# Performance work log

Measured on AMD Instinct MI355X. Metric: run time of the kernel, lower is better.

## Reference

```python
import jax, jax.numpy as jnp
import numpy as np

H = 2048       # hidden_size
NH = 16        # num query heads
NKV = 4        # num key/value heads
HD = 128       # head_dim
EPS = 1e-6
ROPE_BASE = 10000.0


def rms_norm(x, w):
    xf = x.astype(jnp.float32)
    var = jnp.mean(xf * xf, axis=-1, keepdims=True)
    return (w * (xf * jax.lax.rsqrt(var + EPS)).astype(x.dtype))


def rope_cos_sin(seq_len, dtype):
    inv_freq = 1.0 / (ROPE_BASE ** (jnp.arange(0, HD, 2, dtype=jnp.float32) / HD))
    pos = jnp.arange(seq_len, dtype=jnp.float32)
    ang = pos[:, None] * inv_freq[None, :]            # [S, HD/2]
    emb = jnp.concatenate([ang, ang], axis=-1)        # [S, HD]
    return jnp.cos(emb).astype(dtype), jnp.sin(emb).astype(dtype)


def rotate_half(x):
    x1, x2 = jnp.split(x, 2, axis=-1)
    return jnp.concatenate([-x2, x1], axis=-1)


def setup_inputs() -> dict:
    key = jax.random.key(0)
    ks = jax.random.split(key, 8)
    B, S = 2, 2048
    hidden_states = jax.random.normal(ks[0], (B, S, H), dtype=jnp.float32)
    # additive causal mask [B,1,S,S]
    causal = jnp.where(jnp.tril(jnp.ones((S, S), dtype=bool)), 0.0, -1e9).astype(jnp.float32)
    attention_mask = jnp.broadcast_to(causal[None, None], (B, 1, S, S))
    sc = 1.0 / np.sqrt(H)
    Wq = jax.random.normal(ks[1], (NH * HD, H), dtype=jnp.float32) * sc
    Wk = jax.random.normal(ks[2], (NKV * HD, H), dtype=jnp.float32) * sc
    Wv = jax.random.normal(ks[3], (NKV * HD, H), dtype=jnp.float32) * sc
    Wo = jax.random.normal(ks[4], (H, NH * HD), dtype=jnp.float32) * sc
    q_norm_w = jnp.ones((HD,), dtype=jnp.float32)
    k_norm_w = jnp.ones((HD,), dtype=jnp.float32)
    return {"hidden_states": hidden_states, "attention_mask": attention_mask,
            "Wq": Wq, "Wk": Wk, "Wv": Wv, "Wo": Wo,
            "q_norm_w": q_norm_w, "k_norm_w": k_norm_w}


def reference(hidden_states, attention_mask, Wq, Wk, Wv, Wo, q_norm_w, k_norm_w):
    B, S, _ = hidden_states.shape
    # projections (nn.Linear: x @ W.T)
    q = (hidden_states @ Wq.T).reshape(B, S, NH, HD).transpose(0, 2, 1, 3)   # [B,NH,S,HD]
    k = (hidden_states @ Wk.T).reshape(B, S, NKV, HD).transpose(0, 2, 1, 3)  # [B,NKV,S,HD]
    v = (hidden_states @ Wv.T).reshape(B, S, NKV, HD).transpose(0, 2, 1, 3)
    # QK RMSNorm over head_dim
    q = rms_norm(q, q_norm_w)
    k = rms_norm(k, k_norm_w)
    # RoPE
    cos, sin = rope_cos_sin(S, q.dtype)        # [S,HD]
    q = q * cos + rotate_half(q) * sin
    k = k * cos + rotate_half(k) * sin
    # GQA: repeat kv heads
    n_rep = NH // NKV
    k = jnp.repeat(k, n_rep, axis=1)           # [B,NH,S,HD]
    v = jnp.repeat(v, n_rep, axis=1)
    # attention
    scores = jnp.einsum('bhqd,bhkd->bhqk', q, k) / np.sqrt(HD)
    scores = scores + attention_mask
    probs = jax.nn.softmax(scores, axis=-1)
    attn = jnp.einsum('bhqk,bhkd->bhqd', probs, v)
    attn = attn.transpose(0, 2, 1, 3).reshape(B, S, NH * HD)
    return attn @ Wo.T
```

## Files before the change

kernel.cpp:

```cpp
#include <hip/hip_runtime.h>
#include <hip/hip_bf16.h>
#include <math.h>

#define NH 16
#define NKV 4
#define HD 128
#define SEQ 2048
#define BATCH 2
#define EPSF 1e-6f
#define QKV 3072

typedef __attribute__((ext_vector_type(8))) short bf16x8;
typedef __attribute__((ext_vector_type(4))) short short4v;
typedef __attribute__((ext_vector_type(4))) float f32x4;

__device__ __forceinline__ short f2bf(float x) {
    unsigned u = __float_as_uint(x);
    u += 0x7fffu + ((u >> 16) & 1u);
    return (short)(u >> 16);
}
__device__ __forceinline__ float bf2f(short x) {
    return __uint_as_float((unsigned)(unsigned short)x << 16);
}
__device__ __forceinline__ unsigned pkbf(float a, float b) {
    __hip_bfloat162 h = __float22bfloat162_rn(float2{a, b});
    unsigned r; __builtin_memcpy(&r, &h, 4); return r;
}

__device__ __forceinline__ void gll16(const short* g, short* l) {
    __builtin_amdgcn_global_load_lds(
        (const __attribute__((address_space(1))) unsigned*)g,
        (__attribute__((address_space(3))) unsigned*)l, 16, 0, 0);
}

__global__ __launch_bounds__(256)
void cast_all(const float* __restrict__ hs, const float* __restrict__ Wq,
              const float* __restrict__ Wk, const float* __restrict__ Wv,
              const float* __restrict__ Wo, short* __restrict__ hsb,
              short* __restrict__ wqkv, short* __restrict__ wob,
              float2* __restrict__ rtab)
{
    const size_t MEG = 1024 * 1024;
    const int id = blockIdx.x;
    if (id >= 18432) {
        const int idx = (id - 18432) * 256 + threadIdx.x;
        const int s = idx >> 6, j = idx & 63;
        const float inv_freq = exp2f(-(float)j * (13.287712379549449f / 64.0f));
        const float ang = (float)s * inv_freq;
        float sn, c;
        __sincosf(ang, &sn, &c);
        rtab[idx] = float2{c, sn};
        return;
    }
    const float* s;
    short* d;
    size_t off;
    if (id < 8192)       { s = hs; d = hsb;            off = (size_t)id * 1024; }
    else if (id < 12288) { s = Wq; d = wqkv;           off = (size_t)(id - 8192) * 1024; }
    else if (id < 13312) { s = Wk; d = wqkv + 4 * MEG; off = (size_t)(id - 12288) * 1024; }
    else if (id < 14336) { s = Wv; d = wqkv + 5 * MEG; off = (size_t)(id - 13312) * 1024; }
    else                 { s = Wo; d = wob;            off = (size_t)(id - 14336) * 1024; }
    const size_t i = off + threadIdx.x * 4;
    float4 v = *(const float4*)(s + i);
    short4v o;
    o.x = f2bf(v.x); o.y = f2bf(v.y); o.z = f2bf(v.z); o.w = f2bf(v.w);
    *(short4v*)(d + i) = o;
}

template<bool OUT_BF16>
__global__ __launch_bounds__(256, 4)
void gemm_nt_mfma(const short* __restrict__ A, const short* __restrict__ B,
                  void* __restrict__ Cv, int N, int K, int gridX, int total)
{
    __shared__ short As[128 * 64];
    __shared__ short Bs[128 * 64];

    const int tid = threadIdx.x;
    const int w = tid >> 6, lane = tid & 63;
    const int quad = lane >> 4, ln = lane & 15;
    const int mw = (w >> 1) * 64, nw = (w & 1) * 64;

    const int id = blockIdx.x;
    const int t = (id & 7) * (total >> 3) + (id >> 3);
    const int n0 = (t % gridX) * 128;
    const int m0 = (t / gridX) * 128;

    const int rr = lane >> 3;
    const int gsw = ((lane & 7) ^ rr) * 8;
    const short* Ag[4]; const short* Bg[4];
    short* Al[4]; short* Bl[4];
    #pragma unroll
    for (int r = 0; r < 4; ++r) {
        const int row = w * 8 + 32 * r + rr;
        Ag[r] = A + (size_t)(m0 + row) * K + gsw;
        Bg[r] = B + (size_t)(n0 + row) * K + gsw;
        Al[r] = &As[(w * 8 + 32 * r) * 64];
        Bl[r] = &Bs[(w * 8 + 32 * r) * 64];
    }

    const int col0 = ((quad) ^ (ln & 7)) * 8;
    const int col1 = ((4 + quad) ^ (ln & 7)) * 8;

    f32x4 acc[4][4];
    #pragma unroll
    for (int i = 0; i < 4; ++i)
        #pragma unroll
        for (int j = 0; j < 4; ++j)
            acc[i][j] = (f32x4){0.f, 0.f, 0.f, 0.f};

    for (int k0 = 0; k0 < K; k0 += 64) {
        __syncthreads();
        #pragma unroll
        for (int r = 0; r < 4; ++r) {
            gll16(Ag[r] + k0, Al[r]);
            gll16(Bg[r] + k0, Bl[r]);
        }
        __syncthreads();

        #pragma unroll
        for (int ks = 0; ks < 2; ++ks) {
            const int col = ks ? col1 : col0;
            bf16x8 af[4], bfr[4];
            #pragma unroll
            for (int i = 0; i < 4; ++i)
                af[i] = *(const bf16x8*)&As[(mw + i * 16 + ln) * 64 + col];
            #pragma unroll
            for (int j = 0; j < 4; ++j)
                bfr[j] = *(const bf16x8*)&Bs[(nw + j * 16 + ln) * 64 + col];
            #pragma unroll
            for (int i = 0; i < 4; ++i)
                #pragma unroll
                for (int j = 0; j < 4; ++j)
                    acc[i][j] = __builtin_amdgcn_mfma_f32_16x16x32_bf16(
                        af[i], bfr[j], acc[i][j], 0, 0, 0);
        }
    }

    #pragma unroll
    for (int i = 0; i < 4; ++i) {
        #pragma unroll
        for (int reg = 0; reg < 4; ++reg) {
            const int row = m0 + mw + i * 16 + quad * 4 + reg;
            const size_t base = (size_t)row * N + n0 + nw;
            #pragma unroll
            for (int j = 0; j < 4; ++j) {
                if (OUT_BF16)
                    ((short*)Cv)[base + j * 16 + ln] = f2bf(acc[i][j][reg]);
                else
                    ((float*)Cv)[base + j * 16 + ln] = acc[i][j][reg];
            }
        }
    }
}

#define NR_BLOCKS 20480
__global__ __launch_bounds__(256)
void norm_rope_tv(short* __restrict__ qkv, const float* __restrict__ qw,
                  const float* __restrict__ kw, short* __restrict__ vT,
                  const float2* __restrict__ rtab)
{
    if (blockIdx.x < NR_BLOCKS) {
        const int wave = threadIdx.x >> 6;
        const int lane = threadIdx.x & 63;
        const long vec = (long)blockIdx.x * 4 + wave;
        const long NQ = (long)BATCH * SEQ * NH;

        short* base;
        const float* w;
        int s;
        if (vec < NQ) {
            const long token = vec / NH;
            const int h = (int)(vec % NH);
            s = (int)(token % SEQ);
            base = qkv + token * QKV + h * HD;
            w = qw;
        } else {
            const long t = vec - NQ;
            const long token = t / NKV;
            const int kvh = (int)(t % NKV);
            s = (int)(token % SEQ);
            base = qkv + token * QKV + 2048 + kvh * HD;
            w = kw;
        }

        float x0 = bf2f(base[lane]);
        float x1 = bf2f(base[lane + 64]);
        float ss = x0 * x0 + x1 * x1;
        #pragma unroll
        for (int off = 32; off; off >>= 1) ss += __shfl_xor(ss, off, 64);
        const float r = rsqrtf(ss * (1.0f / HD) + EPSF);
        x0 = x0 * r * w[lane];
        x1 = x1 * r * w[lane + 64];

        const float2 cs = rtab[(size_t)s * 64 + lane];
        base[lane]      = f2bf(x0 * cs.x - x1 * cs.y);
        base[lane + 64] = f2bf(x1 * cs.x + x0 * cs.y);
    } else {
        __shared__ short T[32][33];
        const int bx = blockIdx.x - NR_BLOCKS;
        const int st = bx & 63;
        const int dt = (bx >> 6) & 3;
        const int bk = bx >> 8;
        const int s0 = st * 32, d0 = dt * 32;
        const int tid = threadIdx.x;
        const long tok0 = (long)(bk >> 2) * SEQ + s0;
        const int kvh = bk & 3;

        const int rs = tid >> 3;
        const int rc = (tid & 7) * 4;
        short4v val = *(const short4v*)(qkv + (tok0 + rs) * QKV + 2560 + kvh * HD + d0 + rc);
        T[rc + 0][rs] = val.x; T[rc + 1][rs] = val.y;
        T[rc + 2][rs] = val.z; T[rc + 3][rs] = val.w;
        __syncthreads();

        const int wd = tid >> 3;
        const int wsc = (tid & 7) * 4;
        short4v ov;
        ov.x = T[wd][wsc + 0]; ov.y = T[wd][wsc + 1];
        ov.z = T[wd][wsc + 2]; ov.w = T[wd][wsc + 3];
        *(short4v*)(vT + ((size_t)bk * HD + d0 + wd) * SEQ + s0 + wsc) = ov;
    }
}

__global__ __launch_bounds__(512, 4)
void flash_attn_mfma(const short* __restrict__ qkv, const short* __restrict__ vT,
                     short* __restrict__ o)
{
    __shared__ short Ks[64 * 128];
    __shared__ short Vt[128 * 64];
    __shared__ short Ps[8][16 * 64];

    const int tid = threadIdx.x;
    const int w = tid >> 6;
    const int lane = tid & 63;
    const int quad = lane >> 4;
    const int ln = lane & 15;
    const int lnm = ln & 7;
    const int side = w >> 2;
    const int sw = w & 3;

    const int bx = blockIdx.x;
    const int pair = bx & 15;
    const int bh = bx >> 4;
    const int h = bh & 15;
    const int b = bh >> 4;
    const int kvh = h >> 2;
    const int qa = pair, qb = 31 - pair;
    const int qX = side ? qb : qa;
    const int rX = qX * 64 + sw * 16;

    const float SC = 0.08838834764831845f * 1.4426950408889634f;

    int colK[4];
    #pragma unroll
    for (int f = 0; f < 4; ++f) {
        const int lg = f * 4 + quad;
        colK[f] = ((lg & 8) | ((lg ^ lnm) & 7)) * 8;
    }
    const int colA = (quad ^ lnm) * 8;
    const int colB = ((4 + quad) ^ lnm) * 8;

    bf16x8 qf[4];
    {
        const short* qrow = qkv + (size_t)(b * SEQ + rX + ln) * QKV + h * HD;
        #pragma unroll
        for (int f = 0; f < 4; ++f)
            qf[f] = *(const bf16x8*)(qrow + f * 32 + quad * 8);
    }

    f32x4 Oa[8];
    #pragma unroll
    for (int dg = 0; dg < 8; ++dg) Oa[dg] = (f32x4){0.f, 0.f, 0.f, 0.f};
    float mX = -1e30f, lX = 0.f;

    const short* kbase = qkv + (size_t)(b * SEQ) * QKV + 2048 + kvh * HD;
    const short* vbase = vT + (size_t)(b * NKV + kvh) * HD * SEQ;

    bf16x8 kp[2], vp[2];
    auto prefetch = [&](int k0) {
        #pragma unroll
        for (int i = 0; i < 2; ++i) {
            const int e = tid + i * 512;
            kp[i] = *(const bf16x8*)(kbase + (size_t)(k0 + (e >> 4)) * QKV + (e & 15) * 8);
            vp[i] = *(const bf16x8*)(vbase + (size_t)(e >> 3) * SEQ + k0 + (e & 7) * 8);
        }
    };
    prefetch(0);

    for (int kt = 0; kt <= qb; ++kt) {
        const int k0 = kt * 64;
        __syncthreads();
        #pragma unroll
        for (int i = 0; i < 2; ++i) {
            const int e = tid + i * 512;
            const int kr = e >> 4, kg = e & 15;
            *(bf16x8*)&Ks[kr * 128 + ((kg & 8) | ((kg ^ (kr & 7)) & 7)) * 8] = kp[i];
            const int vd = e >> 3, vg = e & 7;
            *(bf16x8*)&Vt[vd * 64 + ((vg ^ (vd & 7)) * 8)] = vp[i];
        }
        __syncthreads();
        if (kt < qb) prefetch(k0 + 64);

        if (kt <= qX) {
            f32x4 s[4];
            __builtin_amdgcn_s_setprio(1);
            #pragma unroll
            for (int g = 0; g < 4; ++g) {
                f32x4 acc = (f32x4){0.f, 0.f, 0.f, 0.f};
                #pragma unroll
                for (int f = 0; f < 4; ++f) {
                    bf16x8 kf = *(const bf16x8*)&Ks[(g * 16 + ln) * 128 + colK[f]];
                    acc = __builtin_amdgcn_mfma_f32_16x16x32_bf16(kf, qf[f], acc, 0, 0, 0);
                }
                s[g] = acc;
            }
            __builtin_amdgcn_s_setprio(0);
            if (kt == qX) {
                const int qrow = rX + ln;
                #pragma unroll
                for (int g = 0; g < 4; ++g)
                    #pragma unroll
                    for (int reg = 0; reg < 4; ++reg) {
                        const int key = k0 + g * 16 + quad * 4 + reg;
                        if (key > qrow) s[g][reg] = -1e30f;
                    }
            }
            float mt = s[0][0];
            #pragma unroll
            for (int g = 0; g < 4; ++g)
                #pragma unroll
                for (int reg = 0; reg < 4; ++reg)
                    mt = fmaxf(mt, s[g][reg]);
            mt = fmaxf(mt, __shfl_xor(mt, 16, 64));
            mt = fmaxf(mt, __shfl_xor(mt, 32, 64));
            const float mnew = fmaxf(mX, mt);
            const bool defer = __all((mnew - mX) * SC <= 6.0f);
            const float mref = defer ? mX : mnew;
            const float c1 = SC * mref;
            const float alpha = exp2f(__builtin_fmaf(SC, mX, -c1));
            float ps = 0.f;
            #pragma unroll
            for (int g = 0; g < 4; ++g) {
                float p0 = exp2f(__builtin_fmaf(s[g][0], SC, -c1));
                float p1 = exp2f(__builtin_fmaf(s[g][1], SC, -c1));
                float p2 = exp2f(__builtin_fmaf(s[g][2], SC, -c1));
                float p3 = exp2f(__builtin_fmaf(s[g][3], SC, -c1));
                ps += (p0 + p1) + (p2 + p3);
                uint2 pk;
                pk.x = pkbf(p0, p1);
                pk.y = pkbf(p2, p3);
                const int sg = (2 * g + (quad >> 1)) ^ lnm;
                *(uint2*)&Ps[w][ln * 64 + sg * 8 + (quad & 1) * 4] = pk;
            }
            ps += __shfl_xor(ps, 16, 64);
            ps += __shfl_xor(ps, 32, 64);
            mX = mref;
            if (defer) {
                lX += ps;
            } else {
                lX = lX * alpha + ps;
                #pragma unroll
                for (int dg = 0; dg < 8; ++dg) {
                    Oa[dg][0] *= alpha; Oa[dg][1] *= alpha;
                    Oa[dg][2] *= alpha; Oa[dg][3] *= alpha;
                }
            }
            __asm volatile("s_waitcnt lgkmcnt(0)" ::: "memory");
            bf16x8 pf0 = *(const bf16x8*)&Ps[w][ln * 64 + colA];
            bf16x8 pf1 = *(const bf16x8*)&Ps[w][ln * 64 + colB];
            __builtin_amdgcn_s_setprio(1);
            #pragma unroll
            for (int dg = 0; dg < 8; ++dg) {
                bf16x8 vf0 = *(const bf16x8*)&Vt[(dg * 16 + ln) * 64 + colA];
                bf16x8 vf1 = *(const bf16x8*)&Vt[(dg * 16 + ln) * 64 + colB];
                Oa[dg] = __builtin_amdgcn_mfma_f32_16x16x32_bf16(vf0, pf0, Oa[dg], 0, 0, 0);
                Oa[dg] = __builtin_amdgcn_mfma_f32_16x16x32_bf16(vf1, pf1, Oa[dg], 0, 0, 0);
            }
            __builtin_amdgcn_s_setprio(0);
        }
    }

    {
        const float inv = 1.0f / lX;
        short* orow = o + ((size_t)(b * SEQ + rX + ln) * NH + h) * HD;
        #pragma unroll
        for (int dg = 0; dg < 8; ++dg) {
            uint2 ov;
            ov.x = pkbf(Oa[dg][0] * inv, Oa[dg][1] * inv);
            ov.y = pkbf(Oa[dg][2] * inv, Oa[dg][3] * inv);
            *(uint2*)(orow + dg * 16 + quad * 4) = ov;
        }
    }
}

extern "C" void kernel_launch(void* const* d_in, const int* in_sizes, int n_in,
                              void* d_out, int out_size, void* d_ws, size_t ws_size,
                              hipStream_t stream)
{
    const float* hs = (const float*)d_in[0];
    const float* Wq = (const float*)d_in[2];
    const float* Wk = (const float*)d_in[3];
    const float* Wv = (const float*)d_in[4];
    const float* Wo = (const float*)d_in[5];
    const float* qw = (const float*)d_in[6];
    const float* kw = (const float*)d_in[7];
    float* out = (float*)d_out;

    const size_t MEG = 1024 * 1024;
    short* hsb  = (short*)d_ws;
    short* wqkv = hsb + 8 * MEG;
    short* wob  = wqkv + 6 * MEG;
    short* qkvb = wob + 4 * MEG;
    float2* rtab = (float2*)(qkvb + 12 * MEG);
    short* vT   = (short*)d_out;

    dim3 blk(256);

    cast_all<<<dim3(18944), blk, 0, stream>>>(hs, Wq, Wk, Wv, Wo, hsb, wqkv, wob, rtab);

    gemm_nt_mfma<true><<<dim3(768), blk, 0, stream>>>(
        hsb, wqkv, qkvb, QKV, 2048, 24, 768);

    norm_rope_tv<<<dim3(NR_BLOCKS + 2048), blk, 0, stream>>>(qkvb, qw, kw, vT, rtab);

    flash_attn_mfma<<<dim3(512), dim3(512), 0, stream>>>(qkvb, vT, hsb);

    gemm_nt_mfma<false><<<dim3(512), blk, 0, stream>>>(
        hsb, wob, out, 2048, 2048, 16, 512);
}
```

Before: 320.5 us.

## Fuse QK RMSNorm and RoPE into QKV GEMM epilogue

The QKV projection GEMM is split into its own kernel whose warps each own 32 full rows by 128 columns, which is one head per tile. That layout lets the epilogue compute the per-head RMS norm with in-wave shuffles and apply RoPE before writing bf16. This removes the separate norm/rope pass, which reread and rewrote Q and K in global memory. The V transpose becomes its own small kernel. The cost is a changed warp tiling (2x8 accumulators, reloaded B fragments) and a heavier epilogue with strided rtab loads, which may affect GEMM efficiency.

Result: no change. 319.1 us (-0.4%).

```diff
diff --git a/kernel.cpp b/kernel.cpp
--- a/kernel.cpp
+++ b/kernel.cpp
@@ -67,18 +67,19 @@
     *(short4v*)(d + i) = o;
 }
 
-template<bool OUT_BF16>
 __global__ __launch_bounds__(256, 4)
-void gemm_nt_mfma(const short* __restrict__ A, const short* __restrict__ B,
-                  void* __restrict__ Cv, int N, int K, int gridX, int total)
+void gemm_qkv(const short* __restrict__ A, const short* __restrict__ B,
+              short* __restrict__ C, const float* __restrict__ qw,
+              const float* __restrict__ kw, const float2* __restrict__ rtab)
 {
+    const int K = 2048, gridX = 24, total = 768;
     __shared__ short As[128 * 64];
     __shared__ short Bs[128 * 64];
 
     const int tid = threadIdx.x;
     const int w = tid >> 6, lane = tid & 63;
     const int quad = lane >> 4, ln = lane & 15;
-    const int mw = (w >> 1) * 64, nw = (w & 1) * 64;
+    const int lnm = ln & 7;
 
     const int id = blockIdx.x;
     const int t = (id & 7) * (total >> 3) + (id >> 3);
@@ -98,14 +99,14 @@
         Bl[r] = &Bs[(w * 8 + 32 * r) * 64];
     }
 
-    const int col0 = ((quad) ^ (ln & 7)) * 8;
-    const int col1 = ((4 + quad) ^ (ln & 7)) * 8;
-
-    f32x4 acc[4][4];
-    #pragma unroll
-    for (int i = 0; i < 4; ++i)
-        #pragma unroll
-        for (int j = 0; j < 4; ++j)
+    const int col0 = ((quad) ^ lnm) * 8;
+    const int col1 = ((4 + quad) ^ lnm) * 8;
+
+    f32x4 acc[2][8];
+    #pragma unroll
+    for (int i = 0; i < 2; ++i)
+        #pragma unroll
+        for (int j = 0; j < 8; ++j)
             acc[i][j] = (f32x4){0.f, 0.f, 0.f, 0.f};
 
     for (int k0 = 0; k0 < K; k0 += 64) {
@@ -120,6 +121,131 @@
         #pragma unroll
         for (int ks = 0; ks < 2; ++ks) {
             const int col = ks ? col1 : col0;
+            bf16x8 af[2], bq[4];
+            af[0] = *(const bf16x8*)&As[(w * 32 + ln) * 64 + col];
+            af[1] = *(const bf16x8*)&As[(w * 32 + 16 + ln) * 64 + col];
+            #pragma unroll
+            for (int j = 0; j < 4; ++j)
+                bq[j] = *(const bf16x8*)&Bs[(j * 16 + ln) * 64 + col];
+            #pragma unroll
+            for (int i = 0; i < 2; ++i)
+                #pragma unroll
+                for (int j = 0; j < 4; ++j)
+                    acc[i][j] = __builtin_amdgcn_mfma_f32_16x16x32_bf16(
+                        af[i], bq[j], acc[i][j], 0, 0, 0);
+            #pragma unroll
+            for (int j = 0; j < 4; ++j)
+                bq[j] = *(const bf16x8*)&Bs[((j + 4) * 16 + ln) * 64 + col];
+            #pragma unroll
+            for (int i = 0; i < 2; ++i)
+                #pragma unroll
+                for (int j = 0; j < 4; ++j)
+                    acc[i][j + 4] = __builtin_amdgcn_mfma_f32_16x16x32_bf16(
+                        af[i], bq[j], acc[i][j + 4], 0, 0, 0);
+        }
+    }
+
+    const int tn = n0 >> 7;
+    const int rowbase = m0 + w * 32;
+
+    if (tn < 20) {
+        const float* wgt = (tn < 16) ? qw : kw;
+        float wv[8];
+        #pragma unroll
+        for (int j = 0; j < 8; ++j) wv[j] = wgt[j * 16 + ln];
+        #pragma unroll
+        for (int i = 0; i < 2; ++i) {
+            #pragma unroll
+            for (int reg = 0; reg < 4; ++reg) {
+                const int row = rowbase + i * 16 + quad * 4 + reg;
+                const int s = row & (SEQ - 1);
+                float ss = 0.f;
+                #pragma unroll
+                for (int j = 0; j < 8; ++j)
+                    ss += acc[i][j][reg] * acc[i][j][reg];
+                ss += __shfl_xor(ss, 1, 64);
+                ss += __shfl_xor(ss, 2, 64);
+                ss += __shfl_xor(ss, 4, 64);
+                ss += __shfl_xor(ss, 8, 64);
+                const float r = rsqrtf(ss * (1.0f / HD) + EPSF);
+                short* orow = C + (size_t)row * QKV + n0;
+                #pragma unroll
+                for (int j = 0; j < 4; ++j) {
+                    const float xlo = acc[i][j][reg] * r * wv[j];
+                    const float xhi = acc[i][j + 4][reg] * r * wv[j + 4];
+                    const float2 cs = rtab[(size_t)s * 64 + j * 16 + ln];
+                    orow[j * 16 + ln]        = f2bf(xlo * cs.x - xhi * cs.y);
+                    orow[(j + 4) * 16 + ln]  = f2bf(xhi * cs.x + xlo * cs.y);
+                }
+            }
+        }
+    } else {
+        #pragma unroll
+        for (int i = 0; i < 2; ++i) {
+            #pragma unroll
+            for (int reg = 0; reg < 4; ++reg) {
+                const int row = rowbase + i * 16 + quad * 4 + reg;
+                short* orow = C + (size_t)row * QKV + n0;
+                #pragma unroll
+                for (int j = 0; j < 8; ++j)
+                    orow[j * 16 + ln] = f2bf(acc[i][j][reg]);
+            }
+        }
+    }
+}
+
+__global__ __launch_bounds__(256, 4)
+void gemm_nt_mfma(const short* __restrict__ A, const short* __restrict__ B,
+                  float* __restrict__ Cv, int N, int K, int gridX, int total)
+{
+    __shared__ short As[128 * 64];
+    __shared__ short Bs[128 * 64];
+
+    const int tid = threadIdx.x;
+    const int w = tid >> 6, lane = tid & 63;
+    const int quad = lane >> 4, ln = lane & 15;
+    const int mw = (w >> 1) * 64, nw = (w & 1) * 64;
+
+    const int id = blockIdx.x;
+    const int t = (id & 7) * (total >> 3) + (id >> 3);
+    const int n0 = (t % gridX) * 128;
+    const int m0 = (t / gridX) * 128;
+
+    const int rr = lane >> 3;
+    const int gsw = ((lane & 7) ^ rr) * 8;
+    const short* Ag[4]; const short* Bg[4];
+    short* Al[4]; short* Bl[4];
+    #pragma unroll
+    for (int r = 0; r < 4; ++r) {
+        const int row = w * 8 + 32 * r + rr;
+        Ag[r] = A + (size_t)(m0 + row) * K + gsw;
+        Bg[r] = B + (size_t)(n0 + row) * K + gsw;
+        Al[r] = &As[(w * 8 + 32 * r) * 64];
+        Bl[r] = &Bs[(w * 8 + 32 * r) * 64];
+    }
+
+    const int col0 = ((quad) ^ (ln & 7)) * 8;
+    const int col1 = ((4 + quad) ^ (ln & 7)) * 8;
+
+    f32x4 acc[4][4];
+    #pragma unroll
+    for (int i = 0; i < 4; ++i)
+        #pragma unroll
+        for (int j = 0; j < 4; ++j)
+            acc[i][j] = (f32x4){0.f, 0.f, 0.f, 0.f};
+
+    for (int k0 = 0; k0 < K; k0 += 64) {
+        __syncthreads();
+        #pragma unroll
+        for (int r = 0; r < 4; ++r) {
+            gll16(Ag[r] + k0, Al[r]);
+            gll16(Bg[r] + k0, Bl[r]);
+        }
+        __syncthreads();
+
+        #pragma unroll
+        for (int ks = 0; ks < 2; ++ks) {
+            const int col = ks ? col1 : col0;
             bf16x8 af[4], bfr[4];
             #pragma unroll
             for (int i = 0; i < 4; ++i)
@@ -143,83 +269,38 @@
             const int row = m0 + mw + i * 16 + quad * 4 + reg;
             const size_t base = (size_t)row * N + n0 + nw;
             #pragma unroll
-            for (int j = 0; j < 4; ++j) {
-                if (OUT_BF16)
-                    ((short*)Cv)[base + j * 16 + ln] = f2bf(acc[i][j][reg]);
-                else
-                    ((float*)Cv)[base + j * 16 + ln] = acc[i][j][reg];
-            }
-        }
-    }
-}
-
-#define NR_BLOCKS 20480
+            for (int j = 0; j < 4; ++j)
+                Cv[base + j * 16 + ln] = acc[i][j][reg];
+        }
+    }
+}
+
 __global__ __launch_bounds__(256)
-void norm_rope_tv(short* __restrict__ qkv, const float* __restrict__ qw,
-                  const float* __restrict__ kw, short* __restrict__ vT,
-                  const float2* __restrict__ rtab)
+void transpose_v(const short* __restrict__ qkv, short* __restrict__ vT)
 {
-    if (blockIdx.x < NR_BLOCKS) {
-        const int wave = threadIdx.x >> 6;
-        const int lane = threadIdx.x & 63;
-        const long vec = (long)blockIdx.x * 4 + wave;
-        const long NQ = (long)BATCH * SEQ * NH;
-
-        short* base;
-        const float* w;
-        int s;
-        if (vec < NQ) {
-            const long token = vec / NH;
-            const int h = (int)(vec % NH);
-            s = (int)(token % SEQ);
-            base = qkv + token * QKV + h * HD;
-            w = qw;
-        } else {
-            const long t = vec - NQ;
-            const long token = t / NKV;
-            const int kvh = (int)(t % NKV);
-            s = (int)(token % SEQ);
-            base = qkv + token * QKV + 2048 + kvh * HD;
-            w = kw;
-        }
-
-        float x0 = bf2f(base[lane]);
-        float x1 = bf2f(base[lane + 64]);
-        float ss = x0 * x0 + x1 * x1;
-        #pragma unroll
-        for (int off = 32; off; off >>= 1) ss += __shfl_xor(ss, off, 64);
-        const float r = rsqrtf(ss * (1.0f / HD) + EPSF);
-        x0 = x0 * r * w[lane];
-        x1 = x1 * r * w[lane + 64];
-
-        const float2 cs = rtab[(size_t)s * 64 + lane];
-        base[lane]      = f2bf(x0 * cs.x - x1 * cs.y);
-        base[lane + 64] = f2bf(x1 * cs.x + x0 * cs.y);
-    } else {
-        __shared__ short T[32][33];
-        const int bx = blockIdx.x - NR_BLOCKS;
-        const int st = bx & 63;
-        const int dt = (bx >> 6) & 3;
-        const int bk = bx >> 8;
-        const int s0 = st * 32, d0 = dt * 32;
-        const int tid = threadIdx.x;
-        const long tok0 = (long)(bk >> 2) * SEQ + s0;
-        const int kvh = bk & 3;
-
-        const int rs = tid >> 3;
-        const int rc = (tid & 7) * 4;
-        short4v val = *(const short4v*)(qkv + (tok0 + rs) * QKV + 2560 + kvh * HD + d0 + rc);
-        T[rc + 0][rs] = val.x; T[rc + 1][rs] = val.y;
-        T[rc + 2][rs] = val.z; T[rc + 3][rs] = val.w;
-        __syncthreads();
-
-        const int wd = tid >> 3;
-        const int wsc = (tid & 7) * 4;
-        short4v ov;
-        ov.x = T[wd][wsc + 0]; ov.y = T[wd][wsc + 1];
-        ov.z = T[wd][wsc + 2]; ov.w = T[wd][wsc + 3];
-        *(short4v*)(vT + ((size_t)bk * HD + d0 + wd) * SEQ + s0 + wsc) = ov;
-    }
+    __shared__ short T[32][33];
+    const int bx = blockIdx.x;
+    const int st = bx & 63;
+    const int dt = (bx >> 6) & 3;
+    const int bk = bx >> 8;
+    const int s0 = st * 32, d0 = dt * 32;
+    const int tid = threadIdx.x;
+    const long tok0 = (long)(bk >> 2) * SEQ + s0;
+    const int kvh = bk & 3;
+
+    const int rs = tid >> 3;
+    const int rc = (tid & 7) * 4;
+    short4v val = *(const short4v*)(qkv + (tok0 + rs) * QKV + 2560 + kvh * HD + d0 + rc);
+    T[rc + 0][rs] = val.x; T[rc + 1][rs] = val.y;
+    T[rc + 2][rs] = val.z; T[rc + 3][rs] = val.w;
+    __syncthreads();
+
+    const int wd = tid >> 3;
+    const int wsc = (tid & 7) * 4;
+    short4v ov;
+    ov.x = T[wd][wsc + 0]; ov.y = T[wd][wsc + 1];
+    ov.z = T[wd][wsc + 2]; ov.w = T[wd][wsc + 3];
+    *(short4v*)(vT + ((size_t)bk * HD + d0 + wd) * SEQ + s0 + wsc) = ov;
 }
 
 __global__ __launch_bounds__(512, 4)
@@ -418,13 +499,12 @@
 
     cast_all<<<dim3(18944), blk, 0, stream>>>(hs, Wq, Wk, Wv, Wo, hsb, wqkv, wob, rtab);
 
-    gemm_nt_mfma<true><<<dim3(768), blk, 0, stream>>>(
-        hsb, wqkv, qkvb, QKV, 2048, 24, 768);
-
-    norm_rope_tv<<<dim3(NR_BLOCKS + 2048), blk, 0, stream>>>(qkvb, qw, kw, vT, rtab);
+    gemm_qkv<<<dim3(768), blk, 0, stream>>>(hsb, wqkv, qkvb, qw, kw, rtab);
+
+    transpose_v<<<dim3(2048), blk, 0, stream>>>(qkvb, vT);
 
     flash_attn_mfma<<<dim3(512), dim3(512), 0, stream>>>(qkvb, vT, hsb);
 
-    gemm_nt_mfma<false><<<dim3(512), blk, 0, stream>>>(
+    gemm_nt_mfma<<<dim3(512), blk, 0, stream>>>(
         hsb, wob, out, 2048, 2048, 16, 512);
 }
```
